# Kernel optimization log

Measured on AMD Instinct MI355X. Metric: run time of the kernel, lower is better.

The kernel has to match this reference:

```python
import jax, jax.numpy as jnp
import numpy as np

B, C, COUT, HEADS = 1, 256, 256, 8
H, W, KS = 96, 96, 7  # spatial dims and neighborhood kernel size


def _nbr_1d(n, k):
    # NATTEN/flex-mask style clamped window: center = clip(q, wl, n-1-wr)
    wl = k // 2
    wr = k // 2 + (k % 2 - 1)
    q = np.arange(n)
    center = np.clip(q, wl, n - 1 - wr)
    start = center - wl  # in [0, n-k]; window always fully in-bounds
    return start[:, None] + np.arange(k)[None, :]  # [n, k]


def _nbr_idx(h, w, k):
    ih = _nbr_1d(h, k)  # [h, k]
    iw = _nbr_1d(w, k)  # [w, k]
    flat = ih[:, None, :, None] * w + iw[None, :, None, :]  # [h, w, k, k]
    return jnp.asarray(flat.reshape(h * w, k * k))  # [S, K]


def setup_inputs() -> dict:
    key = jax.random.key(0)
    ks = jax.random.split(key, 4)
    x = jax.random.normal(ks[0], (B, C, H, W), jnp.float32)
    w_qkv = jax.random.normal(ks[1], (3 * C, C), jnp.float32) * (C ** -0.5)
    b_qkv = jnp.zeros((3 * C,), jnp.float32)
    w_out = jax.random.normal(ks[2], (COUT, C), jnp.float32) * (C ** -0.5)
    b_out = jnp.zeros((COUT,), jnp.float32)
    return {"x": x, "w_qkv": w_qkv, "b_qkv": b_qkv, "w_out": w_out, "b_out": b_out}


def reference(x, w_qkv, b_qkv, w_out, b_out):
    dh = C // HEADS
    S = H * W
    xl = jnp.moveaxis(x, 1, -1)  # [B,H,W,C]
    qkv = xl @ w_qkv.T + b_qkv  # [B,H,W,3C], layout (qkv, heads, dh) on last axis
    qkv = qkv.reshape(B, S, 3, HEADS, dh)
    q = jnp.transpose(qkv[:, :, 0], (0, 2, 1, 3))  # [B,heads,S,dh]
    k = jnp.transpose(qkv[:, :, 1], (0, 2, 1, 3))
    v = jnp.transpose(qkv[:, :, 2], (0, 2, 1, 3))
    # rope_embed_fraction = 0.0 -> RoPE is identity
    nbr = _nbr_idx(H, W, KS)  # [S, K] static neighbor indices, K = KS*KS
    k_nb = jnp.take(k, nbr, axis=2)  # [B,heads,S,K,dh]
    v_nb = jnp.take(v, nbr, axis=2)  # [B,heads,S,K,dh]
    scores = jnp.einsum('bhsd,bhskd->bhsk', q, k_nb) * (dh ** -0.5)
    attn = jax.nn.softmax(scores, axis=-1)  # window fully in-bounds -> no mask
    out = jnp.einsum('bhsk,bhskd->bhsd', attn, v_nb)  # [B,heads,S,dh]
    out = jnp.transpose(out, (0, 2, 1, 3)).reshape(B, S, HEADS * dh)
    out = out @ w_out.T + b_out  # [B,S,COUT]
    out = out.reshape(B, H, W, COUT)
    return jnp.moveaxis(out, -1, 1)  # [B,COUT,H,W]
```

## Files before the change

### kernel.cpp

```cpp
#include <hip/hip_runtime.h>
#include <hip/hip_bf16.h>
#include <math.h>

#define SD 9216
#define HH 96
#define CC 256
#define NO 768
#define NH 8
#define DH 32
#define NW1 (NO * CC)
#define NWT (NW1 + CC * CC)
#define PROW 232

typedef short bf16x8 __attribute__((ext_vector_type(8)));
typedef short short8v __attribute__((ext_vector_type(8)));
typedef float f32x4 __attribute__((ext_vector_type(4)));
typedef unsigned short us8 __attribute__((ext_vector_type(8)));

__device__ __forceinline__ float bf2f(unsigned short u) {
  union { unsigned u; float f; } c; c.u = ((unsigned)u) << 16; return c.f;
}
__device__ __forceinline__ unsigned short f2bf(float f) {
  unsigned u = __float_as_uint(f);
  unsigned r = (u + 0x7FFF + ((u >> 16) & 1)) >> 16;
  return (unsigned short)r;
}
__device__ __forceinline__ void gll16(const unsigned short* g, short* l) {
  __builtin_amdgcn_global_load_lds(
      (const __attribute__((address_space(1))) void*)g,
      (__attribute__((address_space(3))) void*)l, 16, 0, 0);
}

__global__ __launch_bounds__(256) void prep(const float* __restrict__ x,
                                            const float* __restrict__ wq,
                                            const float* __restrict__ wo,
                                            unsigned short* __restrict__ xbt,
                                            unsigned short* __restrict__ wdst) {
  __shared__ float tile[32][33];
  const int b = blockIdx.x;
  const int t = threadIdx.x;
  if (b < 2304) {
    const int s0 = (b % 288) * 32;
    const int c0 = (b / 288) * 32;
    {
      const int c = t >> 3, s4 = (t & 7) * 4;
      const float4 v = *(const float4*)(x + (size_t)(c0 + c) * SD + s0 + s4);
      tile[c][s4] = v.x; tile[c][s4 + 1] = v.y; tile[c][s4 + 2] = v.z; tile[c][s4 + 3] = v.w;
    }
    __syncthreads();
    {
      const int s = t >> 3, c4 = (t & 7) * 4;
      ushort4 o;
      o.x = f2bf(tile[c4][s]);     o.y = f2bf(tile[c4 + 1][s]);
      o.z = f2bf(tile[c4 + 2][s]); o.w = f2bf(tile[c4 + 3][s]);
      *(ushort4*)(xbt + (size_t)(s0 + s) * CC + c0 + c4) = o;
    }
  } else {
    const int i = ((b - 2304) * 256 + t) * 4;
    if (i < NWT) {
      const float* src = (i < NW1) ? (wq + i) : (wo + (i - NW1));
      const float4 v = *(const float4*)src;
      ushort4 o;
      o.x = f2bf(v.x); o.y = f2bf(v.y); o.z = f2bf(v.z); o.w = f2bf(v.w);
      *(ushort4*)(wdst + i) = o;
    }
  }
}

template <int BM, int BN, int EPI>
__global__ __launch_bounds__(256) void gemm_gll(const unsigned short* __restrict__ A,
                                                const unsigned short* __restrict__ Bm,
                                                const float* __restrict__ bias,
                                                void* __restrict__ out) {
  constexpr int MI = BM / 32, NJ = BN / 32;
  __shared__ short Asd[BM * 64];
  __shared__ short Bsd[BN * 64];
  const int t = threadIdx.x;
  const int lane = t & 63;
  const int w = t >> 6;
  const int m0 = blockIdx.x * BM;
  const int n0 = blockIdx.y * BN;
  const int wm = (w >> 1) * (BM / 2);
  const int wn = (w & 1) * (BN / 2);
  f32x4 acc[MI][NJ] = {};
  const int l8 = lane >> 3;
  const int sl = lane & 7;

  for (int k0 = 0; k0 < CC; k0 += 64) {
#pragma unroll
    for (int q = 0; q < BM / 32; ++q) {
      const int r = w * (BM / 4) + q * 8 + l8;
      const int cs = sl ^ (r & 7);
      gll16(A + (size_t)(m0 + r) * CC + k0 + cs * 8, Asd + (w * (BM / 4) + q * 8) * 64);
    }
#pragma unroll
    for (int q = 0; q < BN / 32; ++q) {
      const int r = w * (BN / 4) + q * 8 + l8;
      const int cs = sl ^ (r & 7);
      gll16(Bm + (size_t)(n0 + r) * CC + k0 + cs * 8, Bsd + (w * (BN / 4) + q * 8) * 64);
    }
    __syncthreads();
    const int lr = lane & 15, g = lane >> 4;
#pragma unroll
    for (int kk = 0; kk < 2; ++kk) {
      bf16x8 af[MI], bf[NJ];
#pragma unroll
      for (int i = 0; i < MI; ++i) {
        const int row = wm + i * 16 + lr;
        af[i] = *(const bf16x8*)&Asd[row * 64 + ((kk * 4 + g) ^ (lr & 7)) * 8];
      }
#pragma unroll
      for (int j = 0; j < NJ; ++j) {
        const int row = wn + j * 16 + lr;
        bf[j] = *(const bf16x8*)&Bsd[row * 64 + ((kk * 4 + g) ^ (lr & 7)) * 8];
      }
#pragma unroll
      for (int i = 0; i < MI; ++i)
#pragma unroll
        for (int j = 0; j < NJ; ++j)
          acc[i][j] = __builtin_amdgcn_mfma_f32_16x16x32_bf16(af[i], bf[j], acc[i][j], 0, 0, 0);
    }
    __syncthreads();
  }

  const int lc = lane & 15, lr4 = (lane >> 4) * 4;
  if (EPI == 0) {
    unsigned short* O = (unsigned short*)out;
#pragma unroll
    for (int i = 0; i < MI; ++i)
#pragma unroll
      for (int j = 0; j < NJ; ++j) {
        const int oo = n0 + wn + j * 16 + lc;
        const float bb = bias[oo];
#pragma unroll
        for (int r = 0; r < 4; ++r) {
          const int ss = m0 + wm + i * 16 + lr4 + r;
          O[(size_t)ss * NO + oo] = f2bf(acc[i][j][r] + bb);
        }
      }
  } else {
    float* O = (float*)out;
#pragma unroll
    for (int i = 0; i < MI; ++i)
#pragma unroll
      for (int j = 0; j < NJ; ++j) {
#pragma unroll
        for (int r = 0; r < 4; ++r) {
          const int oo = m0 + wm + i * 16 + lr4 + r;
          const int ss = n0 + wn + j * 16 + lc;
          O[(size_t)oo * SD + ss] = acc[i][j][r] + bias[oo];
        }
      }
  }
}

__global__ __launch_bounds__(256) void nattn_mfma(const unsigned short* __restrict__ qkv,
                                                  unsigned short* __restrict__ att) {
  __shared__ short Vt[32][PROW];
  __shared__ short Ps[4][16][PROW];
  const int t = threadIdx.x;
  const int lane = t & 63;
  const int w = t >> 6;
  const int g = lane >> 4;
  const int qcol = lane & 15;
  const int tile = blockIdx.x;
  const int h = blockIdx.y;
  const int ti = tile / 12, tj = tile % 12;
  const int qi0 = ti * 8, qj0 = tj * 8;
  const int ri0 = min(max(qi0, 3), 92) - 3;
  const int cj0 = min(max(qj0, 3), 92) - 3;

  if (t < 224) {
    const int kg4 = t >> 2, dg = t & 3, d0 = dg * 8;
    unsigned short vv[4][8];
#pragma unroll
    for (int kk = 0; kk < 4; ++kk) {
      const int ku = kg4 * 4 + kk;
      if (ku < 196) {
        const unsigned ru = (unsigned)ku / 14u, cu = (unsigned)ku % 14u;
        const int ur = min(ri0 + (int)ru, 95), uc = min(cj0 + (int)cu, 95);
        const us8 vrow = *(const us8*)(qkv + (size_t)(ur * HH + uc) * NO + 2 * CC + h * DH + d0);
#pragma unroll
        for (int jj = 0; jj < 8; ++jj) vv[kk][jj] = vrow[jj];
      } else {
#pragma unroll
        for (int jj = 0; jj < 8; ++jj) vv[kk][jj] = 0;
      }
    }
#pragma unroll
    for (int jj = 0; jj < 8; ++jj) {
      ushort4 o; o.x = vv[0][jj]; o.y = vv[1][jj]; o.z = vv[2][jj]; o.w = vv[3][jj];
      *(ushort4*)&Vt[d0 + jj][kg4 * 4] = o;
    }
  }

  const int ql = w * 16 + qcol;
  const int qi = qi0 + (ql >> 3), qj = qj0 + (ql & 7);
  const int dr = min(max(qi, 3), 92) - 3 - ri0;
  const int dc = min(max(qj, 3), 92) - 3 - cj0;

  const bf16x8 qf = *(const bf16x8*)(qkv + (size_t)(qi * HH + qj) * NO + h * DH + g * 8);

  f32x4 c[13];
#pragma unroll
  for (int m = 0; m < 13; ++m) {
    const int ku = min(16 * m + qcol, 195);
    const unsigned ru = (unsigned)ku / 14u, cu = (unsigned)ku % 14u;
    const int ur = min(ri0 + (int)ru, 95), uc = min(cj0 + (int)cu, 95);
    const bf16x8 kf = *(const bf16x8*)(qkv + (size_t)(ur * HH + uc) * NO + CC + h * DH + g * 8);
    c[m] = __builtin_amdgcn_mfma_f32_16x16x32_bf16(kf, qf, (f32x4){0.f, 0.f, 0.f, 0.f}, 0, 0, 0);
  }

  float mx = -1e30f;
#pragma unroll
  for (int m = 0; m < 13; ++m)
#pragma unroll
    for (int r = 0; r < 4; ++r) {
      const int ku = 16 * m + 4 * g + r;
      const unsigned ru = (unsigned)ku / 14u, cu = (unsigned)ku % 14u;
      const bool ok = (ku < 196) && ((unsigned)((int)ru - dr) <= 6u) && ((unsigned)((int)cu - dc) <= 6u);
      const float s = ok ? c[m][r] * 0.17677669529663687f : -1e30f;
      c[m][r] = s;
      mx = fmaxf(mx, s);
    }
  mx = fmaxf(mx, __shfl_xor(mx, 16));
  mx = fmaxf(mx, __shfl_xor(mx, 32));
  float sum = 0.f;
#pragma unroll
  for (int m = 0; m < 13; ++m)
#pragma unroll
    for (int r = 0; r < 4; ++r) { const float p = __expf(c[m][r] - mx); c[m][r] = p; sum += p; }
  sum += __shfl_xor(sum, 16);
  sum += __shfl_xor(sum, 32);
  const float inv = 1.0f / sum;

#pragma unroll
  for (int m = 0; m < 13; ++m) {
    ushort4 pk;
    pk.x = f2bf(c[m][0] * inv); pk.y = f2bf(c[m][1] * inv);
    pk.z = f2bf(c[m][2] * inv); pk.w = f2bf(c[m][3] * inv);
    *(ushort4*)&Ps[w][qcol][16 * m + 4 * g] = pk;
  }
  if (lane < 32) {
    const short8v z = {0, 0, 0, 0, 0, 0, 0, 0};
    *(short8v*)&Ps[w][lane >> 1][208 + (lane & 1) * 8] = z;
  }
  __syncthreads();

  f32x4 o0 = {0.f, 0.f, 0.f, 0.f}, o1 = {0.f, 0.f, 0.f, 0.f};
#pragma unroll
  for (int tt = 0; tt < 7; ++tt) {
    const bf16x8 pa = *(const bf16x8*)&Ps[w][qcol][tt * 32 + g * 8];
    const bf16x8 v0 = *(const bf16x8*)&Vt[qcol][tt * 32 + g * 8];
    const bf16x8 v1 = *(const bf16x8*)&Vt[16 + qcol][tt * 32 + g * 8];
    o0 = __builtin_amdgcn_mfma_f32_16x16x32_bf16(pa, v0, o0, 0, 0, 0);
    o1 = __builtin_amdgcn_mfma_f32_16x16x32_bf16(pa, v1, o1, 0, 0, 0);
  }

#pragma unroll
  for (int r = 0; r < 4; ++r) {
    const int qlr = w * 16 + g * 4 + r;
    const int s = (qi0 + (qlr >> 3)) * HH + qj0 + (qlr & 7);
    unsigned short* ap = att + (size_t)s * CC + h * DH;
    ap[qcol] = f2bf(o0[r]);
    ap[16 + qcol] = f2bf(o1[r]);
  }
}

extern "C" void kernel_launch(void* const* d_in, const int* in_sizes, int n_in,
                              void* d_out, int out_size, void* d_ws, size_t ws_size,
                              hipStream_t stream) {
  const float* x     = (const float*)d_in[0];
  const float* w_qkv = (const float*)d_in[1];
  const float* b_qkv = (const float*)d_in[2];
  const float* w_out = (const float*)d_in[3];
  const float* b_out = (const float*)d_in[4];
  float* out = (float*)d_out;

  unsigned short* ws   = (unsigned short*)d_ws;
  unsigned short* xbt  = ws;
  unsigned short* wqb  = xbt + (size_t)SD * CC;
  unsigned short* wob  = wqb + (size_t)NO * CC;
  unsigned short* qkvb = wob + (size_t)CC * CC;
  unsigned short* attb = qkvb + (size_t)SD * NO;

  prep<<<dim3(2304 + NWT / 4 / 256), dim3(256), 0, stream>>>(x, w_qkv, w_out, xbt, wqb);

  gemm_gll<128, 128, 0><<<dim3(SD / 128, NO / 128), dim3(256), 0, stream>>>(xbt, wqb, b_qkv, qkvb);

  nattn_mfma<<<dim3(144, NH), dim3(256), 0, stream>>>(qkvb, attb);

  gemm_gll<64, 128, 1><<<dim3(CC / 64, SD / 128), dim3(256), 0, stream>>>(wob, attb, b_out, out);
}
```

Measured before the change: 108.0 us.

## Stage GEMM epilogues through LDS for coalesced stores; precompute attention gather offsets

Both GEMM epilogues now write accumulators into a shared-memory tile, reusing the staging buffer, and then emit coalesced 16-byte vector stores to global memory instead of scattered scalar stores. This matters most for the transposed fp32 output GEMM. In the attention kernel, neighbor row offsets are computed once into LDS and shared by the K and V gathers. The V loads are issued early into registers and only transposed into LDS after softmax, so their latency overlaps the QK and softmax work. The cost is an extra barrier, some extra LDS traffic, and more register pressure from holding V values.

```diff
diff --git a/kernel.cpp b/kernel.cpp
--- a/kernel.cpp
+++ b/kernel.cpp
@@ -73,8 +73,12 @@
                                                 const float* __restrict__ bias,
                                                 void* __restrict__ out) {
   constexpr int MI = BM / 32, NJ = BN / 32;
-  __shared__ short Asd[BM * 64];
-  __shared__ short Bsd[BN * 64];
+  constexpr int STAGE_SH = (BM + BN) * 64;
+  constexpr int CT_SH = (EPI == 0) ? BM * (BN + 8) : 2 * BM * (BN + 4);
+  constexpr int SMEM_SH = STAGE_SH > CT_SH ? STAGE_SH : CT_SH;
+  __shared__ __align__(16) short smem[SMEM_SH];
+  short* Asd = smem;
+  short* Bsd = smem + BM * 64;
   const int t = threadIdx.x;
   const int lane = t & 63;
   const int w = t >> 6;
@@ -126,36 +130,51 @@
   const int lc = lane & 15, lr4 = (lane >> 4) * 4;
   if (EPI == 0) {
     unsigned short* O = (unsigned short*)out;
+    unsigned short* Ct = (unsigned short*)smem;
 #pragma unroll
     for (int i = 0; i < MI; ++i)
 #pragma unroll
       for (int j = 0; j < NJ; ++j) {
-        const int oo = n0 + wn + j * 16 + lc;
-        const float bb = bias[oo];
+        const float bb = bias[n0 + wn + j * 16 + lc];
+#pragma unroll
+        for (int r = 0; r < 4; ++r)
+          Ct[(wm + i * 16 + lr4 + r) * (BN + 8) + wn + j * 16 + lc] = f2bf(acc[i][j][r] + bb);
+      }
+    __syncthreads();
+#pragma unroll
+    for (int rep = 0; rep < BM * BN / 8 / 256; ++rep) {
+      const int c = rep * 256 + t;
+      const int lrow = c / (BN / 8), lcol8 = (c % (BN / 8)) * 8;
+      *(us8*)(O + (size_t)(m0 + lrow) * NO + n0 + lcol8) =
+          *(const us8*)&Ct[lrow * (BN + 8) + lcol8];
+    }
+  } else {
+    float* O = (float*)out;
+    float* Cf = (float*)smem;
+#pragma unroll
+    for (int i = 0; i < MI; ++i)
+#pragma unroll
+      for (int j = 0; j < NJ; ++j) {
 #pragma unroll
         for (int r = 0; r < 4; ++r) {
-          const int ss = m0 + wm + i * 16 + lr4 + r;
-          O[(size_t)ss * NO + oo] = f2bf(acc[i][j][r] + bb);
+          const int lrow = wm + i * 16 + lr4 + r;
+          Cf[lrow * (BN + 4) + wn + j * 16 + lc] = acc[i][j][r] + bias[m0 + lrow];
         }
       }
-  } else {
-    float* O = (float*)out;
-#pragma unroll
-    for (int i = 0; i < MI; ++i)
-#pragma unroll
-      for (int j = 0; j < NJ; ++j) {
-#pragma unroll
-        for (int r = 0; r < 4; ++r) {
-          const int oo = m0 + wm + i * 16 + lr4 + r;
-          const int ss = n0 + wn + j * 16 + lc;
-          O[(size_t)oo * SD + ss] = acc[i][j][r] + bias[oo];
-        }
-      }
+    __syncthreads();
+#pragma unroll
+    for (int rep = 0; rep < BM * BN / 4 / 256; ++rep) {
+      const int c = rep * 256 + t;
+      const int lrow = c / (BN / 4), lcol4 = (c % (BN / 4)) * 4;
+      *(float4*)(O + (size_t)(m0 + lrow) * SD + n0 + lcol4) =
+          *(const float4*)&Cf[lrow * (BN + 4) + lcol4];
+    }
   }
 }
 
 __global__ __launch_bounds__(256) void nattn_mfma(const unsigned short* __restrict__ qkv,
                                                   unsigned short* __restrict__ att) {
+  __shared__ int offs[224];
   __shared__ short Vt[32][PROW];
   __shared__ short Ps[4][16][PROW];
   const int t = threadIdx.x;
@@ -171,43 +190,30 @@
   const int cj0 = min(max(qj0, 3), 92) - 3;
 
   if (t < 224) {
-    const int kg4 = t >> 2, dg = t & 3, d0 = dg * 8;
-    unsigned short vv[4][8];
-#pragma unroll
-    for (int kk = 0; kk < 4; ++kk) {
-      const int ku = kg4 * 4 + kk;
-      if (ku < 196) {
-        const unsigned ru = (unsigned)ku / 14u, cu = (unsigned)ku % 14u;
-        const int ur = min(ri0 + (int)ru, 95), uc = min(cj0 + (int)cu, 95);
-        const us8 vrow = *(const us8*)(qkv + (size_t)(ur * HH + uc) * NO + 2 * CC + h * DH + d0);
-#pragma unroll
-        for (int jj = 0; jj < 8; ++jj) vv[kk][jj] = vrow[jj];
-      } else {
-#pragma unroll
-        for (int jj = 0; jj < 8; ++jj) vv[kk][jj] = 0;
-      }
-    }
-#pragma unroll
-    for (int jj = 0; jj < 8; ++jj) {
-      ushort4 o; o.x = vv[0][jj]; o.y = vv[1][jj]; o.z = vv[2][jj]; o.w = vv[3][jj];
-      *(ushort4*)&Vt[d0 + jj][kg4 * 4] = o;
-    }
+    const int kr = min(t, 195);
+    const int ru = kr / 14, cu = kr - ru * 14;
+    offs[t] = (min(ri0 + ru, 95) * HH + min(cj0 + cu, 95)) * NO;
   }
 
   const int ql = w * 16 + qcol;
   const int qi = qi0 + (ql >> 3), qj = qj0 + (ql & 7);
   const int dr = min(max(qi, 3), 92) - 3 - ri0;
   const int dc = min(max(qj, 3), 92) - 3 - cj0;
-
   const bf16x8 qf = *(const bf16x8*)(qkv + (size_t)(qi * HH + qj) * NO + h * DH + g * 8);
+  __syncthreads();
+
+  us8 vreg[4];
+  const int kg4 = t >> 2, d0 = (t & 3) * 8;
+  if (t < 224) {
+#pragma unroll
+    for (int kk = 0; kk < 4; ++kk)
+      vreg[kk] = *(const us8*)(qkv + (size_t)offs[kg4 * 4 + kk] + 2 * CC + h * DH + d0);
+  }
 
   f32x4 c[13];
 #pragma unroll
   for (int m = 0; m < 13; ++m) {
-    const int ku = min(16 * m + qcol, 195);
-    const unsigned ru = (unsigned)ku / 14u, cu = (unsigned)ku % 14u;
-    const int ur = min(ri0 + (int)ru, 95), uc = min(cj0 + (int)cu, 95);
-    const bf16x8 kf = *(const bf16x8*)(qkv + (size_t)(ur * HH + uc) * NO + CC + h * DH + g * 8);
+    const bf16x8 kf = *(const bf16x8*)(qkv + (size_t)offs[16 * m + qcol] + CC + h * DH + g * 8);
     c[m] = __builtin_amdgcn_mfma_f32_16x16x32_bf16(kf, qf, (f32x4){0.f, 0.f, 0.f, 0.f}, 0, 0, 0);
   }
 
@@ -244,6 +250,15 @@
   if (lane < 32) {
     const short8v z = {0, 0, 0, 0, 0, 0, 0, 0};
     *(short8v*)&Ps[w][lane >> 1][208 + (lane & 1) * 8] = z;
+  }
+
+  if (t < 224) {
+#pragma unroll
+    for (int jj = 0; jj < 8; ++jj) {
+      ushort4 o;
+      o.x = vreg[0][jj]; o.y = vreg[1][jj]; o.z = vreg[2][jj]; o.w = vreg[3][jj];
+      *(ushort4*)&Vt[d0 + jj][kg4 * 4] = o;
+    }
   }
   __syncthreads();
 
```

After: 105.7 us. -2.1%, faster.
